# Kernel tuning notes

Hardware: AMD Instinct MI355X
Metric: run time of the kernel (lower is better)

The kernel has to match this reference:

```python
import jax, jax.numpy as jnp
import numpy as np

D = 1024
B, S_IMG, S_CTX = 2, 4096, 512
EPS = 1e-6


def rmsnorm(x, eps=1e-6):
    return x * jax.lax.rsqrt(jnp.mean(x * x, axis=-1, keepdims=True) + eps)


def layernorm(x, eps=1e-6):
    mu = jnp.mean(x, axis=-1, keepdims=True)
    var = jnp.mean((x - mu) ** 2, axis=-1, keepdims=True)
    return (x - mu) * jax.lax.rsqrt(var + eps)


def act_quant(x):
    # per-token 8-bit absmax quant
    scale = 127.0 / jnp.clip(jnp.max(jnp.abs(x), axis=-1, keepdims=True), 1e-5)
    return jnp.clip(jnp.round(x * scale), -128, 127) / scale


def weight_quant(w):
    # ternary (1.58-bit) absmean quant
    scale = 1.0 / jnp.clip(jnp.mean(jnp.abs(w)), 1e-5)
    return jnp.clip(jnp.round(w * scale), -1, 1) / scale


def bitlinear(x, w):
    # BitNet: RMSNorm -> STE activation quant, STE ternary weight quant
    xn = rmsnorm(x)
    xq = xn + jax.lax.stop_gradient(act_quant(xn) - xn)
    wq = w + jax.lax.stop_gradient(weight_quant(w) - w)
    return jnp.einsum('bsd,od->bso', xq, wq)


def ada_ln_zero(x, emb, w, b):
    e = (jax.nn.silu(emb) @ w.T + b)[:, None, :]  # [B,1,6D]
    scale_msa, shift_msa, gate_msa, scale_mlp, shift_mlp, gate_mlp = jnp.split(e, 6, axis=2)
    xn = layernorm(x) * (1.0 + scale_msa) + shift_msa
    return xn, gate_msa, shift_mlp, scale_mlp, gate_mlp


def hgrn_bit_attention(x, wi, wf, wg, wo, gnorm_w):
    i = bitlinear(x, wi)
    f = jax.nn.sigmoid(bitlinear(x, wf))
    i = jax.nn.silu(i) * (1.0 - f)  # swiglu(i, 1-f)
    # elementwise linear recurrence h_t = f_t * h_{t-1} + i_t over seq dim
    def step(h, xs):
        i_t, f_t = xs
        h = f_t * h + i_t
        return h, h
    _, o = jax.lax.scan(step, jnp.zeros_like(i[:, 0]), (i.transpose(1, 0, 2), f.transpose(1, 0, 2)))
    o = o.transpose(1, 0, 2)  # [B,S,D]
    g = bitlinear(x, wg)
    o = rmsnorm(o) * gnorm_w * (g * jax.nn.sigmoid(g))  # RMSNorm + swish gate
    return bitlinear(o, wo)


def bit_mlp(x, w_gate, w_down):
    y = bitlinear(x, w_gate)
    gate, y = jnp.split(y, 2, axis=-1)
    return bitlinear(jax.nn.silu(gate) * y, w_down)


def flux_block(hidden_states, encoder_hidden_states, temb,
               adaln_w, adaln_b, adaln_ctx_w, adaln_ctx_b,
               attn_wi, attn_wf, attn_wg, attn_wo, attn_gnorm_w,
               ff_wgate, ff_wdown, ffc_wgate, ffc_wdown):
    nh, gate_msa, shift_mlp, scale_mlp, gate_mlp = ada_ln_zero(hidden_states, temb, adaln_w, adaln_b)
    nc, c_gate_msa, c_shift_mlp, c_scale_mlp, c_gate_mlp = ada_ln_zero(encoder_hidden_states, temb, adaln_ctx_w, adaln_ctx_b)
    len_c = nc.shape[1]
    joint = jnp.concatenate([nc, nh], axis=1)
    attn_out = hgrn_bit_attention(joint, attn_wi, attn_wf, attn_wg, attn_wo, attn_gnorm_w)
    c_attn, x_attn = attn_out[:, :len_c], attn_out[:, len_c:]

    hidden_states = hidden_states + gate_msa * x_attn
    nh2 = layernorm(hidden_states) * (1.0 + scale_mlp) + shift_mlp
    hidden_states = hidden_states + gate_mlp * bit_mlp(nh2, ff_wgate, ff_wdown)

    encoder_hidden_states = encoder_hidden_states + c_gate_msa * c_attn
    nc2 = layernorm(encoder_hidden_states) * (1.0 + c_scale_mlp) + c_shift_mlp
    encoder_hidden_states = encoder_hidden_states + c_gate_mlp * bit_mlp(nc2, ffc_wgate, ffc_wdown)
    return hidden_states, encoder_hidden_states


def setup_inputs() -> dict:
    key = jax.random.key(0)
    ks = jax.random.split(key, 16)
    w = lambda k, shape: jax.random.normal(k, shape, jnp.float32) * 0.02
    return {
        'hidden_states': jax.random.normal(ks[0], (B, S_IMG, D), jnp.float32),
        'encoder_hidden_states': jax.random.normal(ks[1], (B, S_CTX, D), jnp.float32),
        'temb': jax.random.normal(ks[2], (B, D), jnp.float32),
        'adaln_w': w(ks[3], (6 * D, D)), 'adaln_b': jnp.zeros((6 * D,), jnp.float32),
        'adaln_ctx_w': w(ks[4], (6 * D, D)), 'adaln_ctx_b': jnp.zeros((6 * D,), jnp.float32),
        'attn_wi': w(ks[5], (D, D)), 'attn_wf': w(ks[6], (D, D)),
        'attn_wg': w(ks[7], (D, D)), 'attn_wo': w(ks[8], (D, D)),
        'attn_gnorm_w': jnp.ones((D,), jnp.float32),
        'ff_wgate': w(ks[9], (8 * D, D)), 'ff_wdown': w(ks[10], (D, 4 * D)),
        'ffc_wgate': w(ks[11], (8 * D, D)), 'ffc_wdown': w(ks[12], (D, 4 * D)),
    }


def reference(hidden_states, encoder_hidden_states, temb,
              adaln_w, adaln_b, adaln_ctx_w, adaln_ctx_b,
              attn_wi, attn_wf, attn_wg, attn_wo, attn_gnorm_w,
              ff_wgate, ff_wdown, ffc_wgate, ffc_wdown):
    return flux_block(hidden_states, encoder_hidden_states, temb,
                      adaln_w, adaln_b, adaln_ctx_w, adaln_ctx_b,
                      attn_wi, attn_wf, attn_wg, attn_wo, attn_gnorm_w,
                      ff_wgate, ff_wdown, ffc_wgate, ffc_wdown)
```

## Files before the change

kernel.cpp:

```cpp
#include <hip/hip_runtime.h>
#include <hip/hip_bf16.h>
#include <stdint.h>

#define DM   1024
#define SJ   4608
#define SCTX 512
#define SIMG 4096
#define NCH  512
#define TCH  9

typedef __attribute__((ext_vector_type(4))) int   i32x4;
typedef __attribute__((ext_vector_type(4))) float f32x4;

__device__ __forceinline__ float bf2f(unsigned short u){
  union { unsigned int i; float f; } v; v.i = ((unsigned int)u) << 16; return v.f;
}
__device__ __forceinline__ unsigned short f2bf(float f){
  unsigned int u = __float_as_uint(f);
  u += 0x7fffu + ((u >> 16) & 1u);
  return (unsigned short)(u >> 16);
}
__device__ __forceinline__ float sigm(float x){ return 1.f/(1.f+__expf(-x)); }
__device__ __forceinline__ signed char q8(float v, float lo, float hi){
  return (signed char)(int)fminf(fmaxf(rintf(v),lo),hi);
}

__device__ __forceinline__ float wsum(float v){
  #pragma unroll
  for(int o=32;o>0;o>>=1) v += __shfl_xor(v,o);
  return v;
}
__device__ __forceinline__ float wmax(float v){
  #pragma unroll
  for(int o=32;o>0;o>>=1) v = fmaxf(v,__shfl_xor(v,o));
  return v;
}
__device__ __forceinline__ void blockSumSum(float& a, float& b, float* s1, float* s2){
  a = wsum(a); b = wsum(b);
  if(!(threadIdx.x&63)){ s1[threadIdx.x>>6]=a; s2[threadIdx.x>>6]=b; }
  __syncthreads();
  a = s1[0]+s1[1]+s1[2]+s1[3];
  b = s2[0]+s2[1]+s2[2]+s2[3];
  __syncthreads();
}
__device__ __forceinline__ void blockSumMax(float& a, float& b, float* s1, float* s2){
  a = wsum(a); b = wmax(b);
  if(!(threadIdx.x&63)){ s1[threadIdx.x>>6]=a; s2[threadIdx.x>>6]=b; }
  __syncthreads();
  a = s1[0]+s1[1]+s1[2]+s1[3];
  b = fmaxf(fmaxf(s2[0],s2[1]),fmaxf(s2[2],s2[3]));
  __syncthreads();
}

typedef __attribute__((address_space(1))) void gvoid_t;
typedef __attribute__((address_space(3))) void lvoid_t;
__device__ __forceinline__ void gl_lds16(const void* g, void* l){
  __builtin_amdgcn_global_load_lds((gvoid_t*)g, (lvoid_t*)l, 16, 0, 0);
}

struct WList {
  const float* w[8];
  unsigned long long n[8];
  signed char* q[8];
};

__global__ __launch_bounds__(256)
void wq_reduce(WList L, float* __restrict__ part){
  __shared__ float s1[4];
  int m = blockIdx.y;
  const float4* w4 = (const float4*)L.w[m];
  size_t n4 = L.n[m] >> 2;
  float s = 0.f;
  for(size_t i = (size_t)blockIdx.x*256 + threadIdx.x; i < n4; i += (size_t)512*256){
    float4 v = w4[i];
    s += fabsf(v.x)+fabsf(v.y)+fabsf(v.z)+fabsf(v.w);
  }
  s = wsum(s);
  if(!(threadIdx.x&63)) s1[threadIdx.x>>6] = s;
  __syncthreads();
  if(!threadIdx.x) part[m*512 + blockIdx.x] = s1[0]+s1[1]+s1[2]+s1[3];
}

__global__ __launch_bounds__(256)
void wq_finalize(WList L, const float* __restrict__ part, float* __restrict__ swinv){
  __shared__ float s1[4];
  int m = blockIdx.x;
  float s = part[m*512 + threadIdx.x] + part[m*512 + 256 + threadIdx.x];
  s = wsum(s);
  if(!(threadIdx.x&63)) s1[threadIdx.x>>6] = s;
  __syncthreads();
  if(!threadIdx.x){
    float mean = (s1[0]+s1[1]+s1[2]+s1[3]) / (float)L.n[m];
    swinv[m] = fmaxf(mean, 1e-5f);
  }
}

__global__ __launch_bounds__(256)
void wq_quant(WList L, const float* __restrict__ swinv){
  int m = blockIdx.y;
  float sc = 1.f / swinv[m];
  const float4* w4 = (const float4*)L.w[m];
  signed char* q = L.q[m];
  size_t n4 = L.n[m] >> 2;
  for(size_t i = (size_t)blockIdx.x*256 + threadIdx.x; i < n4; i += (size_t)1024*256){
    float4 v = w4[i];
    char4 o;
    o.x = q8(v.x*sc,-1.f,1.f);
    o.y = q8(v.y*sc,-1.f,1.f);
    o.z = q8(v.z*sc,-1.f,1.f);
    o.w = q8(v.w*sc,-1.f,1.f);
    ((char4*)q)[i] = o;
  }
}

__global__ __launch_bounds__(256)
void adaln_gemv(const float* __restrict__ temb, const float* __restrict__ W,
                const float* __restrict__ bias, float* __restrict__ e){
  int o = blockIdx.x*4 + (threadIdx.x>>6);
  int b = blockIdx.y;
  int lane = threadIdx.x & 63;
  const float4* t4 = (const float4*)(temb + b*DM);
  const float4* w4 = (const float4*)(W + (size_t)o*DM);
  float acc = 0.f;
  #pragma unroll
  for(int i=0;i<4;i++){
    float4 tv = t4[i*64+lane], wv = w4[i*64+lane];
    acc += (tv.x*sigm(tv.x))*wv.x + (tv.y*sigm(tv.y))*wv.y
         + (tv.z*sigm(tv.z))*wv.z + (tv.w*sigm(tv.w))*wv.w;
  }
  acc = wsum(acc);
  if(!lane) e[b*6144 + o] = acc + bias[o];
}

__global__ __launch_bounds__(256)
void modnorm_quant(const float* __restrict__ x, int bshift,
                   const float* __restrict__ e, int scaleOff, int shiftOff,
                   signed char* __restrict__ xq, float* __restrict__ rsx,
                   int outRowOff, int outBatchStride){
  __shared__ float s1[4], s2[4];
  const int tid = threadIdx.x;
  const int row = blockIdx.x;
  const int b = row >> bshift, s = row & ((1<<bshift)-1);
  float4 xv = ((const float4*)(x + (size_t)row*DM))[tid];
  float sum = xv.x+xv.y+xv.z+xv.w;
  float ss  = xv.x*xv.x+xv.y*xv.y+xv.z*xv.z+xv.w*xv.w;
  blockSumSum(sum, ss, s1, s2);
  float mu  = sum * (1.f/DM);
  float inv = rsqrtf(ss*(1.f/DM) - mu*mu + 1e-6f);
  float4 scv = ((const float4*)(e + b*6144 + scaleOff))[tid];
  float4 shv = ((const float4*)(e + b*6144 + shiftOff))[tid];
  float n0 = (xv.x-mu)*inv*(1.f+scv.x)+shv.x;
  float n1 = (xv.y-mu)*inv*(1.f+scv.y)+shv.y;
  float n2 = (xv.z-mu)*inv*(1.f+scv.z)+shv.z;
  float n3 = (xv.w-mu)*inv*(1.f+scv.w)+shv.w;
  float ss2 = n0*n0+n1*n1+n2*n2+n3*n3;
  float mx  = fmaxf(fmaxf(fabsf(n0),fabsf(n1)),fmaxf(fabsf(n2),fabsf(n3)));
  blockSumMax(ss2, mx, s1, s2);
  float rms   = rsqrtf(ss2*(1.f/DM) + 1e-6f);
  float amaxn = fmaxf(mx*rms, 1e-5f);
  float k     = rms*127.f/amaxn;
  int orow = b*outBatchStride + outRowOff + s;
  char4 q;
  q.x = q8(n0*k,-128.f,127.f);
  q.y = q8(n1*k,-128.f,127.f);
  q.z = q8(n2*k,-128.f,127.f);
  q.w = q8(n3*k,-128.f,127.f);
  ((char4*)(xq + (size_t)orow*DM))[tid] = q;
  if(!tid) rsx[orow] = amaxn*(1.f/127.f);
}

__global__ __launch_bounds__(256)
void gnorm_quant(const unsigned short* __restrict__ o, const unsigned short* __restrict__ g,
                 const float* __restrict__ gnw,
                 signed char* __restrict__ xq, float* __restrict__ rsx){
  __shared__ float s1[4], s2[4];
  const int tid = threadIdx.x;
  const size_t row = blockIdx.x;
  ushort4 ov = ((const ushort4*)(o + row*DM))[tid];
  ushort4 gv = ((const ushort4*)(g + row*DM))[tid];
  float o0=bf2f(ov.x), o1=bf2f(ov.y), o2=bf2f(ov.z), o3=bf2f(ov.w);
  float g0=bf2f(gv.x), g1=bf2f(gv.y), g2=bf2f(gv.z), g3=bf2f(gv.w);
  float ss = o0*o0+o1*o1+o2*o2+o3*o3;
  float dummy = 0.f;
  blockSumSum(ss, dummy, s1, s2);
  float rms = rsqrtf(ss*(1.f/DM) + 1e-6f);
  float4 wv = ((const float4*)gnw)[tid];
  float n0 = o0*rms*wv.x*(g0*sigm(g0));
  float n1 = o1*rms*wv.y*(g1*sigm(g1));
  float n2 = o2*rms*wv.z*(g2*sigm(g2));
  float n3 = o3*rms*wv.w*(g3*sigm(g3));
  float ss2 = n0*n0+n1*n1+n2*n2+n3*n3;
  float mx  = fmaxf(fmaxf(fabsf(n0),fabsf(n1)),fmaxf(fabsf(n2),fabsf(n3)));
  blockSumMax(ss2, mx, s1, s2);
  float rms2  = rsqrtf(ss2*(1.f/DM) + 1e-6f);
  float amaxn = fmaxf(mx*rms2, 1e-5f);
  float k     = rms2*127.f/amaxn;
  char4 q;
  q.x = q8(n0*k,-128.f,127.f);
  q.y = q8(n1*k,-128.f,127.f);
  q.z = q8(n2*k,-128.f,127.f);
  q.w = q8(n3*k,-128.f,127.f);
  ((char4*)(xq + row*DM))[tid] = q;
  if(!tid) rsx[row] = amaxn*(1.f/127.f);
}

__global__ __launch_bounds__(256)
void rmsq4096(const unsigned short* __restrict__ z, signed char* __restrict__ zq,
              float* __restrict__ rsx){
  __shared__ float s1[4], s2[4];
  const int tid = threadIdx.x;
  const unsigned short* zr = z + (size_t)blockIdx.x*4096;
  signed char* qr = zq + (size_t)blockIdx.x*4096;
  float v[16];
  #pragma unroll
  for(int i=0;i<4;i++){
    ushort4 u = ((const ushort4*)zr)[tid + i*256];
    v[i*4+0]=bf2f(u.x); v[i*4+1]=bf2f(u.y); v[i*4+2]=bf2f(u.z); v[i*4+3]=bf2f(u.w);
  }
  float ss=0.f, mx=0.f;
  #pragma unroll
  for(int i=0;i<16;i++){ ss += v[i]*v[i]; mx = fmaxf(mx, fabsf(v[i])); }
  blockSumMax(ss, mx, s1, s2);
  float rms   = rsqrtf(ss*(1.f/4096.f) + 1e-6f);
  float amaxn = fmaxf(mx*rms, 1e-5f);
  float k     = rms*127.f/amaxn;
  #pragma unroll
  for(int i=0;i<4;i++){
    char4 q;
    q.x = q8(v[i*4+0]*k,-128.f,127.f);
    q.y = q8(v[i*4+1]*k,-128.f,127.f);
    q.z = q8(v[i*4+2]*k,-128.f,127.f);
    q.w = q8(v[i*4+3]*k,-128.f,127.f);
    ((char4*)qr)[tid + i*256] = q;
  }
  if(!tid) rsx[blockIdx.x] = amaxn*(1.f/127.f);
}

__global__ __launch_bounds__(256)
void scan_pass1(const unsigned short* __restrict__ ir, const unsigned short* __restrict__ fr,
                float* __restrict__ A, float* __restrict__ B){
  int c = blockIdx.x, b = blockIdx.y;
  int d0 = threadIdx.x*4;
  size_t base = ((size_t)b*SJ + (size_t)c*TCH)*DM + d0;
  float a0=1,a1=1,a2=1,a3=1, h0=0,h1=0,h2=0,h3=0;
  #pragma unroll
  for(int t=0;t<TCH;t++){
    ushort4 iv = *(const ushort4*)(ir + base + (size_t)t*DM);
    ushort4 fv = *(const ushort4*)(fr + base + (size_t)t*DM);
    float f0=sigm(bf2f(fv.x)), f1=sigm(bf2f(fv.y)), f2=sigm(bf2f(fv.z)), f3=sigm(bf2f(fv.w));
    float x0=bf2f(iv.x), x1=bf2f(iv.y), x2=bf2f(iv.z), x3=bf2f(iv.w);
    float p0=x0*sigm(x0)*(1.f-f0), p1=x1*sigm(x1)*(1.f-f1);
    float p2=x2*sigm(x2)*(1.f-f2), p3=x3*sigm(x3)*(1.f-f3);
    h0=f0*h0+p0; h1=f1*h1+p1; h2=f2*h2+p2; h3=f3*h3+p3;
    a0*=f0; a1*=f1; a2*=f2; a3*=f3;
  }
  size_t idx = (size_t)c*2048 + b*1024 + d0;
  *(float4*)(A + idx) = make_float4(a0,a1,a2,a3);
  *(float4*)(B + idx) = make_float4(h0,h1,h2,h3);
}

__global__ __launch_bounds__(256)
void scan_pass2(const float* __restrict__ A, const float* __restrict__ B, float* __restrict__ H){
  int chain = blockIdx.x*256 + threadIdx.x;
  float h = 0.f;
  for(int c0=0;c0<NCH;c0+=8){
    float a[8], bb[8];
    #pragma unroll
    for(int u=0;u<8;u++){
      a[u]  = A[(size_t)(c0+u)*2048 + chain];
      bb[u] = B[(size_t)(c0+u)*2048 + chain];
    }
    #pragma unroll
    for(int u=0;u<8;u++){
      H[(size_t)(c0+u)*2048 + chain] = h;
      h = a[u]*h + bb[u];
    }
  }
}

__global__ __launch_bounds__(256)
void scan_pass3(const unsigned short* __restrict__ ir, const unsigned short* __restrict__ fr,
                const float* __restrict__ H, unsigned short* __restrict__ o){
  int c = blockIdx.x, b = blockIdx.y;
  int d0 = threadIdx.x*4;
  size_t base = ((size_t)b*SJ + (size_t)c*TCH)*DM + d0;
  float4 hv = *(const float4*)(H + (size_t)c*2048 + b*1024 + d0);
  float h0=hv.x, h1=hv.y, h2=hv.z, h3=hv.w;
  #pragma unroll
  for(int t=0;t<TCH;t++){
    ushort4 iv = *(const ushort4*)(ir + base + (size_t)t*DM);
    ushort4 fv = *(const ushort4*)(fr + base + (size_t)t*DM);
    float f0=sigm(bf2f(fv.x)), f1=sigm(bf2f(fv.y)), f2=sigm(bf2f(fv.z)), f3=sigm(bf2f(fv.w));
    float x0=bf2f(iv.x), x1=bf2f(iv.y), x2=bf2f(iv.z), x3=bf2f(iv.w);
    float p0=x0*sigm(x0)*(1.f-f0), p1=x1*sigm(x1)*(1.f-f1);
    float p2=x2*sigm(x2)*(1.f-f2), p3=x3*sigm(x3)*(1.f-f3);
    h0=f0*h0+p0; h1=f1*h1+p1; h2=f2*h2+p2; h3=f3*h3+p3;
    ushort4 ov; ov.x=f2bf(h0); ov.y=f2bf(h1); ov.z=f2bf(h2); ov.w=f2bf(h3);
    *(ushort4*)(o + base + (size_t)t*DM) = ov;
  }
}

#define EPI_IFG    0
#define EPI_WO     1
#define EPI_GLU    2
#define EPI_RESID  3

struct GemmP {
  const float* rsx;
  const float* swinv;
  unsigned short* outb;
  float* outf;
  const float* resid;
  const float* egate;
  int bshift;
  const signed char* w2;
  const float* eh; const float* ec;
  const float* hid; const float* enc;
  float* out_h; float* out_c; float* out_c2;
};

template<int VAR, int EPI, int SWZ>
__global__ __launch_bounds__(512, 2)
void gemm8(const signed char* __restrict__ Aq, const signed char* __restrict__ Bq,
           int Ncols, int K, int lda, GemmP p){
  constexpr int BBYT = (VAR==2)? 16384 : 32768;
  constexpr int TB   = 32768 + BBYT;
  constexpr int NF   = (VAR==0)? 4 : 2;
  constexpr int BN   = (VAR==0)? 256 : 128;
  __shared__ char lds[2*TB];

  const int tid = threadIdx.x, wv = tid>>6, lane = tid&63;
  const int wm = wv>>2, wn = wv&3;
  const int nwg = gridDim.x*gridDim.y;
  const int id  = blockIdx.y*gridDim.x + blockIdx.x;
  int nb, mb;
  if constexpr (SWZ==1){
    const int x = id&7, j = id>>3;
    nb = x*4 + (j&3);
    mb = j>>2;
  } else {
    const int wg = (id&7)*(nwg>>3) + (id>>3);
    nb = wg % gridDim.x; mb = wg / gridDim.x;
  }

  const int srow = wv*8 + (lane>>3);
  const int sch  = ((lane&7) ^ (lane>>3))*16;
  const signed char* ag  = Aq + (size_t)(mb*256 + srow)*lda + sch;
  const signed char* bg1 = Bq + (size_t)(nb*BN  + srow)*lda + sch;
  const signed char* bg2 = nullptr;
  if constexpr (VAR==1) bg2 = p.w2 + (size_t)(nb*128 + srow)*lda + sch;
  const int wvoff = wv*1024;

  auto stageA = [&](char* bufn, int rb, int k0){
    gl_lds16(ag + (size_t)rb*lda + k0, bufn + rb*128 + wvoff);
  };
  auto stageB = [&](char* bufn, int rb, int k0, int m2){
    const signed char* src = m2 ? bg2 : bg1;
    gl_lds16(src + (size_t)rb*lda + k0, bufn + 32768 + m2*16384 + rb*128 + wvoff);
  };
  auto stagePh = [&](int ph, char* bufn, int kn){
    if constexpr (VAR==0){
      if(ph==0){ stageB(bufn,0,kn,0);   stageB(bufn,64,kn,0); }
      else if(ph==1){ stageB(bufn,128,kn,0); stageB(bufn,192,kn,0); }
      else if(ph==2){ stageA(bufn,0,kn);   stageA(bufn,128,kn); }
      else          { stageA(bufn,64,kn);  stageA(bufn,192,kn); }
    } else if constexpr (VAR==1){
      if(ph==0){ stageB(bufn,0,kn,0);  stageB(bufn,64,kn,0); }
      else if(ph==1){ stageB(bufn,0,kn,1);  stageB(bufn,64,kn,1); }
      else if(ph==2){ stageA(bufn,0,kn);   stageA(bufn,128,kn); }
      else          { stageA(bufn,64,kn);  stageA(bufn,192,kn); }
    } else {
      if(ph==0){ stageB(bufn,0,kn,0);  stageB(bufn,64,kn,0); }
      else if(ph==1){ stageA(bufn,0,kn);   stageA(bufn,128,kn); }
      else if(ph==2){ stageA(bufn,64,kn);  stageA(bufn,192,kn); }
    }
  };

  const int lr = lane&15;
  const int kq = lane>>4;
  const int axor = (lr&7)<<4;
  const int col0 = (kq<<4) ^ axor;
  const int col1 = (64 | (kq<<4)) ^ axor;
  const int arowb = (wm*128 + lr)*128;
  const int browb = ((VAR==0? wn*64 : wn*32) + lr)*128;

  i32x4 acc[8][NF];
  i32x4 acc2[(VAR==1)?8:1][NF];
  #pragma unroll
  for(int i=0;i<8;i++)
    #pragma unroll
    for(int j=0;j<NF;j++){ acc[i][j]=(i32x4){0,0,0,0}; if constexpr(VAR==1) acc2[i][j]=(i32x4){0,0,0,0}; }

  i32x4 breg[NF], breg2[(VAR==1)?NF:1];

  auto phase = [&](char* bufc, int ph, char* bufn, int kn, bool doStage){
    const int colb = (ph>>1)? col1 : col0;
    const int mh = ph&1;
    if(mh==0){
      #pragma unroll
      for(int nf=0;nf<NF;nf++)
        breg[nf] = *(const i32x4*)(bufc + 32768 + browb + nf*2048 + colb);
      if constexpr (VAR==1){
        #pragma unroll
        for(int nf=0;nf<NF;nf++)
          breg2[nf] = *(const i32x4*)(bufc + 32768 + 16384 + browb + nf*2048 + colb);
      }
    }
    i32x4 areg[4];
    #pragma unroll
    for(int i=0;i<4;i++)
      areg[i] = *(const i32x4*)(bufc + arowb + (mh*4+i)*2048 + colb);
    if(doStage) stagePh(ph, bufn, kn);
    __builtin_amdgcn_s_setprio(1);
    #pragma unroll
    for(int i=0;i<4;i++){
      #pragma unroll
      for(int nf=0;nf<NF;nf++){
        acc[mh*4+i][nf] = __builtin_amdgcn_mfma_i32_16x16x64_i8(areg[i], breg[nf], acc[mh*4+i][nf], 0,0,0);
        if constexpr (VAR==1)
          acc2[mh*4+i][nf] = __builtin_amdgcn_mfma_i32_16x16x64_i8(areg[i], breg2[nf], acc2[mh*4+i][nf], 0,0,0);
      }
    }
    __builtin_amdgcn_s_setprio(0);
  };

  #define VMW2 asm volatile("s_waitcnt vmcnt(2)" ::: "memory")
  #define VMW0 asm volatile("s_waitcnt vmcnt(0)" ::: "memory")
  #define BARR { __builtin_amdgcn_s_barrier(); __builtin_amdgcn_sched_barrier(0); }

  stagePh(0, lds, 0); stagePh(1, lds, 0); stagePh(2, lds, 0); stagePh(3, lds, 0);

  const int NT = K>>7;
  for(int t=0; t<NT-1; ++t){
    char* bufc = lds + (t&1)*TB;
    char* bufn = lds + ((t+1)&1)*TB;
    const int kn = (t+1)<<7;
    VMW2; BARR; phase(bufc, 0, bufn, kn, true);
    VMW2; BARR; phase(bufc, 1, bufn, kn, true);
          BARR; phase(bufc, 2, bufn, kn, true);
          BARR; phase(bufc, 3, bufn, kn, true);
  }
  {
    char* bufc = lds + ((NT-1)&1)*TB;
    VMW2; BARR; phase(bufc, 0, nullptr, 0, false);
    VMW0; BARR; phase(bufc, 1, nullptr, 0, false);
          BARR; phase(bufc, 2, nullptr, 0, false);
          BARR; phase(bufc, 3, nullptr, 0, false);
  }

  float sw;
  if constexpr (EPI==EPI_IFG) sw = p.swinv[(nb*256)>>10];
  else                        sw = *p.swinv;
  const int r0 = mb*256 + wm*128;
  const int c0 = nb*BN + wn*((VAR==0)?64:32);
  #pragma unroll
  for(int mf=0;mf<8;mf++){
    #pragma unroll
    for(int j=0;j<4;j++){
      int r = r0 + mf*16 + kq*4 + j;
      float rs = p.rsx[r]*sw;
      #pragma unroll
      for(int nf=0;nf<NF;nf++){
        int c = c0 + nf*16 + lr;
        float val = (float)acc[mf][nf][j]*rs;
        if constexpr (EPI==EPI_IFG){
          int mat = c >> 10;
          p.outb[(size_t)mat*9437184 + (size_t)r*1024 + (c&1023)] = f2bf(val);
        } else if constexpr (EPI==EPI_GLU){
          float v2 = (float)acc2[mf][nf][j]*rs;
          p.outb[(size_t)r*Ncols + c] = f2bf(val*sigm(val)*v2);
        } else if constexpr (EPI==EPI_RESID){
          int b = r >> p.bshift;
          size_t idx = (size_t)r*DM + c;
          p.outf[idx] = p.resid[idx] + p.egate[b*6144 + 5*1024 + c]*val;
        } else {
          int b = r / SJ; int s = r - b*SJ;
          if (s < SCTX){
            size_t idx = ((size_t)b*SCTX + s)*DM + c;
            float ov = p.enc[idx] + p.ec[b*6144 + 2*1024 + c]*val;
            p.out_c[idx]  = ov;
            p.out_c2[idx] = ov;
          } else {
            size_t idx = ((size_t)b*SIMG + (s-SCTX))*DM + c;
            p.out_h[idx] = p.hid[idx] + p.eh[b*6144 + 2*1024 + c]*val;
          }
        }
      }
    }
  }
  #undef VMW2
  #undef VMW0
  #undef BARR
}

__global__ __launch_bounds__(256, 2)
void gemm_ra8(const signed char* __restrict__ Aq, const signed char* __restrict__ Wq,
              int K, int lda, GemmP p){
  __shared__ signed char As[128*128];
  __shared__ signed char Bs[128*128];
  const int tid = threadIdx.x;
  const int wave = tid>>6, lane = tid&63;
  const int nwg = gridDim.x*gridDim.y;
  const int id  = blockIdx.y*gridDim.x + blockIdx.x;
  const int wg  = (id&7)*(nwg>>3) + (id>>3);
  const int nb  = wg % gridDim.x, mb = wg / gridDim.x;
  const int wr = wave>>1, wc = wave&1;
  const int koff = blockIdx.z*K;

  const int grow = wave*8 + (lane>>3);
  const int gcol = (lane&7)*16;
  const signed char* ag = Aq + (size_t)(mb*128 + grow)*lda + koff + gcol;
  const signed char* bg = Wq + (size_t)(nb*128 + grow)*lda + koff + gcol;
  char* asl = (char*)As + wave*1024;
  char* bsl = (char*)Bs + wave*1024;

  i32x4 acc[4][4];
  #pragma unroll
  for(int i=0;i<4;i++)
    #pragma unroll
    for(int j=0;j<4;j++) acc[i][j] = (i32x4){0,0,0,0};

  const int lrow = lane&15, kq = lane>>4;
  const signed char* arow = &As[(wr*64 + lrow)*128 + kq*16];
  const signed char* brow = &Bs[(wc*64 + lrow)*128 + kq*16];

  for(int k0=0; k0<K; k0+=128){
    #pragma unroll
    for(int pp=0;pp<4;pp++){
      gl_lds16(ag + (size_t)pp*32*lda + k0, asl + pp*4096);
      gl_lds16(bg + (size_t)pp*32*lda + k0, bsl + pp*4096);
    }
    __syncthreads();
    #pragma unroll
    for(int kk=0;kk<2;kk++){
      i32x4 af[4], bfr[4];
      #pragma unroll
      for(int m=0;m<4;m++) af[m]  = *(const i32x4*)(arow + m*2048 + kk*64);
      #pragma unroll
      for(int n=0;n<4;n++) bfr[n] = *(const i32x4*)(brow + n*2048 + kk*64);
      #pragma unroll
      for(int m=0;m<4;m++)
        #pragma unroll
        for(int n=0;n<4;n++)
          acc[m][n] = __builtin_amdgcn_mfma_i32_16x16x64_i8(af[m], bfr[n], acc[m][n], 0,0,0);
    }
    __syncthreads();
  }

  const float sw = *p.swinv;
  const int r0 = mb*128 + wr*64, c0 = nb*128 + wc*64;
  #pragma unroll
  for(int m=0;m<4;m++){
    #pragma unroll
    for(int j=0;j<4;j++){
      int r = r0 + m*16 + kq*4 + j;
      float rs = p.rsx[r]*sw;
      #pragma unroll
      for(int n=0;n<4;n++){
        int c = c0 + n*16 + lrow;
        float val = (float)acc[m][n][j]*rs;
        int b = r >> p.bshift;
        size_t idx = (size_t)r*DM + c;
        atomicAdd(&p.outf[idx], p.egate[b*6144 + 5*1024 + c]*val);
      }
    }
  }
}

extern "C" void kernel_launch(void* const* d_in, const int* in_sizes, int n_in,
                              void* d_out, int out_size, void* d_ws, size_t ws_size,
                              hipStream_t stream){
  (void)in_sizes; (void)n_in; (void)out_size; (void)ws_size;
  const float* hidden   = (const float*)d_in[0];
  const float* enc      = (const float*)d_in[1];
  const float* temb     = (const float*)d_in[2];
  const float* adaln_w  = (const float*)d_in[3];
  const float* adaln_b  = (const float*)d_in[4];
  const float* adaln_cw = (const float*)d_in[5];
  const float* adaln_cb = (const float*)d_in[6];
  const float* wi  = (const float*)d_in[7];
  const float* wf  = (const float*)d_in[8];
  const float* wg  = (const float*)d_in[9];
  const float* wo  = (const float*)d_in[10];
  const float* gnw = (const float*)d_in[11];
  const float* ffg = (const float*)d_in[12];
  const float* ffd = (const float*)d_in[13];
  const float* fcg = (const float*)d_in[14];
  const float* fcd = (const float*)d_in[15];

  const size_t MB = 1024ull*1024ull;
  char* ws = (char*)d_ws;
  signed char* W8_IFG = (signed char*)(ws + 0*MB);
  signed char* W8_WO  = (signed char*)(ws + 3*MB);
  signed char* W8_FFG = (signed char*)(ws + 4*MB);
  signed char* W8_FFD = (signed char*)(ws + 12*MB);
  signed char* W8_FCG = (signed char*)(ws + 16*MB);
  signed char* W8_FCD = (signed char*)(ws + 24*MB);
  float* PART  = (float*)(ws + 28*MB);
  float* SWINV = (float*)(ws + 28*MB + 32*1024);
  float* EH    = (float*)(ws + 28*MB + 64*1024);
  float* EC    = (float*)(ws + 28*MB + 112*1024);
  float* RSX1  = (float*)(ws + 28*MB + 160*1024);
  float* RSX2  = (float*)(ws + 28*MB + 200*1024);
  float* RSX3  = (float*)(ws + 28*MB + 240*1024);
  float* RSXZ  = (float*)(ws + 28*MB + 280*1024);
  float* RSX4  = (float*)(ws + 28*MB + 320*1024);
  float* RSXZC = (float*)(ws + 28*MB + 328*1024);
  float* SCANA = (float*)(ws + 29*MB);
  float* SCANB = (float*)(ws + 33*MB);
  float* SCANH = (float*)(ws + 37*MB);
  signed char* XQ8 = (signed char*)(ws + 41*MB);
  unsigned short* IRAW = (unsigned short*)(ws + 51*MB);
  unsigned short* FRAW = (unsigned short*)(ws + 69*MB);
  unsigned short* GRAW = (unsigned short*)(ws + 87*MB);
  unsigned short* OBUF = (unsigned short*)(ws + 105*MB);
  unsigned short* SGB  = (unsigned short*)(ws + 51*MB);
  signed char* SG8 = (signed char*)(ws + 115*MB);
  float* HNEW = (float*)(ws + 147*MB);
  float* CNEW = (float*)(ws + 181*MB);
  float* OUT_H = (float*)d_out;
  float* OUT_C = (float*)d_out + 8388608;

  WList L;
  L.w[0]=wi;  L.n[0]=1048576ull; L.q[0]=W8_IFG;
  L.w[1]=wf;  L.n[1]=1048576ull; L.q[1]=W8_IFG + 1048576;
  L.w[2]=wg;  L.n[2]=1048576ull; L.q[2]=W8_IFG + 2097152;
  L.w[3]=wo;  L.n[3]=1048576ull; L.q[3]=W8_WO;
  L.w[4]=ffg; L.n[4]=8388608ull; L.q[4]=W8_FFG;
  L.w[5]=ffd; L.n[5]=4194304ull; L.q[5]=W8_FFD;
  L.w[6]=fcg; L.n[6]=8388608ull; L.q[6]=W8_FCG;
  L.w[7]=fcd; L.n[7]=4194304ull; L.q[7]=W8_FCD;
  wq_reduce  <<<dim3(512,8), 256, 0, stream>>>(L, PART);
  wq_finalize<<<8,          256, 0, stream>>>(L, PART, SWINV);
  wq_quant   <<<dim3(1024,8),256, 0, stream>>>(L, SWINV);

  adaln_gemv<<<dim3(1536,2), 256, 0, stream>>>(temb, adaln_w,  adaln_b,  EH);
  adaln_gemv<<<dim3(1536,2), 256, 0, stream>>>(temb, adaln_cw, adaln_cb, EC);

  modnorm_quant<<<1024, 256, 0, stream>>>(enc,    9,  EC, 0, 1024, XQ8, RSX1, 0,   SJ);
  modnorm_quant<<<8192, 256, 0, stream>>>(hidden, 12, EH, 0, 1024, XQ8, RSX1, 512, SJ);

  GemmP p{};
  p.rsx = RSX1; p.swinv = SWINV; p.outb = IRAW;
  gemm8<0,EPI_IFG,0><<<dim3(12,36), 512, 0, stream>>>(XQ8, W8_IFG, 3072, 1024, 1024, p);

  scan_pass1<<<dim3(NCH,2), 256, 0, stream>>>(IRAW, FRAW, SCANA, SCANB);
  scan_pass2<<<8,           256, 0, stream>>>(SCANA, SCANB, SCANH);
  scan_pass3<<<dim3(NCH,2), 256, 0, stream>>>(IRAW, FRAW, SCANH, OBUF);

  gnorm_quant<<<9216, 256, 0, stream>>>(OBUF, GRAW, gnw, XQ8, RSX2);

  GemmP pw{};
  pw.rsx = RSX2; pw.swinv = SWINV+3;
  pw.eh = EH; pw.ec = EC; pw.hid = hidden; pw.enc = enc;
  pw.out_h = HNEW; pw.out_c = CNEW; pw.out_c2 = OUT_C;
  gemm8<2,EPI_WO,0><<<dim3(8,36), 512, 0, stream>>>(XQ8, W8_WO, 1024, 1024, 1024, pw);

  modnorm_quant<<<8192, 256, 0, stream>>>(HNEW, 12, EH, 3*1024, 4*1024, XQ8, RSX3, 0, SIMG);
  GemmP pg{};
  pg.rsx = RSX3; pg.swinv = SWINV+4; pg.outb = SGB; pg.w2 = W8_FFG + (size_t)4096*1024;
  gemm8<1,EPI_GLU,1><<<dim3(32,32), 512, 0, stream>>>(XQ8, W8_FFG, 4096, 1024, 1024, pg);
  rmsq4096<<<8192, 256, 0, stream>>>(SGB, SG8, RSXZ);
  GemmP pd{};
  pd.rsx = RSXZ; pd.swinv = SWINV+5; pd.outf = OUT_H; pd.resid = HNEW; pd.egate = EH; pd.bshift = 12;
  gemm8<2,EPI_RESID,0><<<dim3(8,32), 512, 0, stream>>>(SG8, W8_FFD, 1024, 4096, 4096, pd);

  modnorm_quant<<<1024, 256, 0, stream>>>(CNEW, 9, EC, 3*1024, 4*1024, XQ8, RSX4, 0, SCTX);
  GemmP pc{};
  pc.rsx = RSX4; pc.swinv = SWINV+6; pc.outb = SGB; pc.w2 = W8_FCG + (size_t)4096*1024;
  gemm8<1,EPI_GLU,1><<<dim3(32,4), 512, 0, stream>>>(XQ8, W8_FCG, 4096, 1024, 1024, pc);
  rmsq4096<<<1024, 256, 0, stream>>>(SGB, SG8, RSXZC);
  GemmP pe{};
  pe.rsx = RSXZC; pe.swinv = SWINV+7; pe.outf = OUT_C; pe.egate = EC; pe.bshift = 9;
  gemm_ra8<<<dim3(8,8,4), 256, 0, stream>>>(SG8, W8_FCD, 1024, 4096, pe);
}
```

Before: 511.4 us.

## Fuse gated RMSNorm into scan pass and move residual adds out of GEMM epilogues

The group-norm/swish-gate/quantization step now runs inside the final scan pass, so the bf16 scan output buffer is never written or reread. The Wo and FF-down GEMMs now write plain bf16 outputs. Their residual-plus-gate adds move into separate elementwise kernels, one of which also does the next adaLN modulated norm and quantization. This shortens the GEMM epilogues, which previously did scattered fp32 reads and writes. In exchange it adds extra bf16 intermediate traffic, two block reductions per timestep inside the scan kernel, and rounds the attention and MLP outputs to bf16 before the residual add.

```diff
diff --git a/kernel.cpp b/kernel.cpp
--- a/kernel.cpp
+++ b/kernel.cpp
@@ -170,38 +170,65 @@
 }
 
 __global__ __launch_bounds__(256)
-void gnorm_quant(const unsigned short* __restrict__ o, const unsigned short* __restrict__ g,
-                 const float* __restrict__ gnw,
-                 signed char* __restrict__ xq, float* __restrict__ rsx){
+void resid_modnorm(const float* __restrict__ x, const unsigned short* __restrict__ attn,
+                   int attnRowOff, int bshift,
+                   const float* __restrict__ e,
+                   float* __restrict__ hout,
+                   signed char* __restrict__ xq, float* __restrict__ rsx){
   __shared__ float s1[4], s2[4];
   const int tid = threadIdx.x;
-  const size_t row = blockIdx.x;
-  ushort4 ov = ((const ushort4*)(o + row*DM))[tid];
-  ushort4 gv = ((const ushort4*)(g + row*DM))[tid];
-  float o0=bf2f(ov.x), o1=bf2f(ov.y), o2=bf2f(ov.z), o3=bf2f(ov.w);
-  float g0=bf2f(gv.x), g1=bf2f(gv.y), g2=bf2f(gv.z), g3=bf2f(gv.w);
-  float ss = o0*o0+o1*o1+o2*o2+o3*o3;
-  float dummy = 0.f;
-  blockSumSum(ss, dummy, s1, s2);
-  float rms = rsqrtf(ss*(1.f/DM) + 1e-6f);
-  float4 wv = ((const float4*)gnw)[tid];
-  float n0 = o0*rms*wv.x*(g0*sigm(g0));
-  float n1 = o1*rms*wv.y*(g1*sigm(g1));
-  float n2 = o2*rms*wv.z*(g2*sigm(g2));
-  float n3 = o3*rms*wv.w*(g3*sigm(g3));
+  const int row = blockIdx.x;
+  const int b = row >> bshift, s = row & ((1<<bshift)-1);
+  const int arow = b*SJ + attnRowOff + s;
+  float4 xv = ((const float4*)(x + (size_t)row*DM))[tid];
+  ushort4 av = ((const ushort4*)(attn + (size_t)arow*DM))[tid];
+  float4 gv = ((const float4*)(e + b*6144 + 2*1024))[tid];
+  float h0 = xv.x + gv.x*bf2f(av.x);
+  float h1 = xv.y + gv.y*bf2f(av.y);
+  float h2 = xv.z + gv.z*bf2f(av.z);
+  float h3 = xv.w + gv.w*bf2f(av.w);
+  ((float4*)(hout + (size_t)row*DM))[tid] = make_float4(h0,h1,h2,h3);
+  float sum = h0+h1+h2+h3;
+  float ss  = h0*h0+h1*h1+h2*h2+h3*h3;
+  blockSumSum(sum, ss, s1, s2);
+  float mu  = sum * (1.f/DM);
+  float inv = rsqrtf(ss*(1.f/DM) - mu*mu + 1e-6f);
+  float4 scv = ((const float4*)(e + b*6144 + 3*1024))[tid];
+  float4 shv = ((const float4*)(e + b*6144 + 4*1024))[tid];
+  float n0 = (h0-mu)*inv*(1.f+scv.x)+shv.x;
+  float n1 = (h1-mu)*inv*(1.f+scv.y)+shv.y;
+  float n2 = (h2-mu)*inv*(1.f+scv.z)+shv.z;
+  float n3 = (h3-mu)*inv*(1.f+scv.w)+shv.w;
   float ss2 = n0*n0+n1*n1+n2*n2+n3*n3;
   float mx  = fmaxf(fmaxf(fabsf(n0),fabsf(n1)),fmaxf(fabsf(n2),fabsf(n3)));
   blockSumMax(ss2, mx, s1, s2);
-  float rms2  = rsqrtf(ss2*(1.f/DM) + 1e-6f);
-  float amaxn = fmaxf(mx*rms2, 1e-5f);
-  float k     = rms2*127.f/amaxn;
+  float rms   = rsqrtf(ss2*(1.f/DM) + 1e-6f);
+  float amaxn = fmaxf(mx*rms, 1e-5f);
+  float k     = rms*127.f/amaxn;
   char4 q;
   q.x = q8(n0*k,-128.f,127.f);
   q.y = q8(n1*k,-128.f,127.f);
   q.z = q8(n2*k,-128.f,127.f);
   q.w = q8(n3*k,-128.f,127.f);
-  ((char4*)(xq + row*DM))[tid] = q;
+  ((char4*)(xq + (size_t)row*DM))[tid] = q;
   if(!tid) rsx[row] = amaxn*(1.f/127.f);
+}
+
+__global__ __launch_bounds__(256)
+void resid_out(const float* __restrict__ hnew, const unsigned short* __restrict__ mlp,
+               const float* __restrict__ e, int bshift, float* __restrict__ out){
+  const int tid = threadIdx.x;
+  const int row = blockIdx.x;
+  const int b = row >> bshift;
+  float4 hv = ((const float4*)(hnew + (size_t)row*DM))[tid];
+  ushort4 mv = ((const ushort4*)(mlp + (size_t)row*DM))[tid];
+  float4 gv = ((const float4*)(e + b*6144 + 5*1024))[tid];
+  float4 o;
+  o.x = hv.x + gv.x*bf2f(mv.x);
+  o.y = hv.y + gv.y*bf2f(mv.y);
+  o.z = hv.z + gv.z*bf2f(mv.z);
+  o.w = hv.w + gv.w*bf2f(mv.w);
+  ((float4*)(out + (size_t)row*DM))[tid] = o;
 }
 
 __global__ __launch_bounds__(256)
@@ -279,13 +306,18 @@
 }
 
 __global__ __launch_bounds__(256)
-void scan_pass3(const unsigned short* __restrict__ ir, const unsigned short* __restrict__ fr,
-                const float* __restrict__ H, unsigned short* __restrict__ o){
+void scan3_gnorm(const unsigned short* __restrict__ ir, const unsigned short* __restrict__ fr,
+                 const float* __restrict__ H, const unsigned short* __restrict__ g,
+                 const float* __restrict__ gnw,
+                 signed char* __restrict__ xq, float* __restrict__ rsx){
+  __shared__ float s1[4], s2[4];
   int c = blockIdx.x, b = blockIdx.y;
-  int d0 = threadIdx.x*4;
+  const int tid = threadIdx.x;
+  int d0 = tid*4;
   size_t base = ((size_t)b*SJ + (size_t)c*TCH)*DM + d0;
   float4 hv = *(const float4*)(H + (size_t)c*2048 + b*1024 + d0);
   float h0=hv.x, h1=hv.y, h2=hv.z, h3=hv.w;
+  float4 wv = ((const float4*)gnw)[tid];
   #pragma unroll
   for(int t=0;t<TCH;t++){
     ushort4 iv = *(const ushort4*)(ir + base + (size_t)t*DM);
@@ -295,28 +327,44 @@
     float p0=x0*sigm(x0)*(1.f-f0), p1=x1*sigm(x1)*(1.f-f1);
     float p2=x2*sigm(x2)*(1.f-f2), p3=x3*sigm(x3)*(1.f-f3);
     h0=f0*h0+p0; h1=f1*h1+p1; h2=f2*h2+p2; h3=f3*h3+p3;
-    ushort4 ov; ov.x=f2bf(h0); ov.y=f2bf(h1); ov.z=f2bf(h2); ov.w=f2bf(h3);
-    *(ushort4*)(o + base + (size_t)t*DM) = ov;
+    float ss = h0*h0+h1*h1+h2*h2+h3*h3, dummy = 0.f;
+    blockSumSum(ss, dummy, s1, s2);
+    float rms = rsqrtf(ss*(1.f/DM) + 1e-6f);
+    ushort4 gv = *(const ushort4*)(g + base + (size_t)t*DM);
+    float g0=bf2f(gv.x), g1=bf2f(gv.y), g2=bf2f(gv.z), g3=bf2f(gv.w);
+    float n0 = h0*rms*wv.x*(g0*sigm(g0));
+    float n1 = h1*rms*wv.y*(g1*sigm(g1));
+    float n2 = h2*rms*wv.z*(g2*sigm(g2));
+    float n3 = h3*rms*wv.w*(g3*sigm(g3));
+    float ss2 = n0*n0+n1*n1+n2*n2+n3*n3;
+    float mx  = fmaxf(fmaxf(fabsf(n0),fabsf(n1)),fmaxf(fabsf(n2),fabsf(n3)));
+    blockSumMax(ss2, mx, s1, s2);
+    float rms2  = rsqrtf(ss2*(1.f/DM) + 1e-6f);
+    float amaxn = fmaxf(mx*rms2, 1e-5f);
+    float k     = rms2*127.f/amaxn;
+    char4 q;
+    q.x = q8(n0*k,-128.f,127.f);
+    q.y = q8(n1*k,-128.f,127.f);
+    q.z = q8(n2*k,-128.f,127.f);
+    q.w = q8(n3*k,-128.f,127.f);
+    size_t row = (size_t)b*SJ + (size_t)c*TCH + t;
+    *(char4*)(xq + row*DM + d0) = q;
+    if(!tid) rsx[row] = amaxn*(1.f/127.f);
   }
 }
 
 #define EPI_IFG    0
-#define EPI_WO     1
+#define EPI_OUT    1
 #define EPI_GLU    2
-#define EPI_RESID  3
 
 struct GemmP {
   const float* rsx;
   const float* swinv;
   unsigned short* outb;
   float* outf;
-  const float* resid;
   const float* egate;
   int bshift;
   const signed char* w2;
-  const float* eh; const float* ec;
-  const float* hid; const float* enc;
-  float* out_h; float* out_c; float* out_c2;
 };
 
 template<int VAR, int EPI, int SWZ>
@@ -469,21 +517,8 @@
         } else if constexpr (EPI==EPI_GLU){
           float v2 = (float)acc2[mf][nf][j]*rs;
           p.outb[(size_t)r*Ncols + c] = f2bf(val*sigm(val)*v2);
-        } else if constexpr (EPI==EPI_RESID){
-          int b = r >> p.bshift;
-          size_t idx = (size_t)r*DM + c;
-          p.outf[idx] = p.resid[idx] + p.egate[b*6144 + 5*1024 + c]*val;
         } else {
-          int b = r / SJ; int s = r - b*SJ;
-          if (s < SCTX){
-            size_t idx = ((size_t)b*SCTX + s)*DM + c;
-            float ov = p.enc[idx] + p.ec[b*6144 + 2*1024 + c]*val;
-            p.out_c[idx]  = ov;
-            p.out_c2[idx] = ov;
-          } else {
-            size_t idx = ((size_t)b*SIMG + (s-SCTX))*DM + c;
-            p.out_h[idx] = p.hid[idx] + p.eh[b*6144 + 2*1024 + c]*val;
-          }
+          p.outb[(size_t)r*Ncols + c] = f2bf(val);
         }
       }
     }
@@ -613,11 +648,11 @@
   unsigned short* IRAW = (unsigned short*)(ws + 51*MB);
   unsigned short* FRAW = (unsigned short*)(ws + 69*MB);
   unsigned short* GRAW = (unsigned short*)(ws + 87*MB);
-  unsigned short* OBUF = (unsigned short*)(ws + 105*MB);
-  unsigned short* SGB  = (unsigned short*)(ws + 51*MB);
-  signed char* SG8 = (signed char*)(ws + 115*MB);
-  float* HNEW = (float*)(ws + 147*MB);
-  float* CNEW = (float*)(ws + 181*MB);
+  unsigned short* ATTN = (unsigned short*)(ws + 51*MB);
+  signed char* SG8 = (signed char*)(ws + 51*MB);
+  unsigned short* MLPH = (unsigned short*)(ws + 83*MB);
+  float* HNEW = (float*)(ws + 105*MB);
+  unsigned short* SGB = (unsigned short*)(ws + 137*MB);
   float* OUT_H = (float*)d_out;
   float* OUT_C = (float*)d_out + 8388608;
 
@@ -646,29 +681,28 @@
 
   scan_pass1<<<dim3(NCH,2), 256, 0, stream>>>(IRAW, FRAW, SCANA, SCANB);
   scan_pass2<<<8,           256, 0, stream>>>(SCANA, SCANB, SCANH);
-  scan_pass3<<<dim3(NCH,2), 256, 0, stream>>>(IRAW, FRAW, SCANH, OBUF);
-
-  gnorm_quant<<<9216, 256, 0, stream>>>(OBUF, GRAW, gnw, XQ8, RSX2);
+  scan3_gnorm<<<dim3(NCH,2), 256, 0, stream>>>(IRAW, FRAW, SCANH, GRAW, gnw, XQ8, RSX2);
 
   GemmP pw{};
-  pw.rsx = RSX2; pw.swinv = SWINV+3;
-  pw.eh = EH; pw.ec = EC; pw.hid = hidden; pw.enc = enc;
-  pw.out_h = HNEW; pw.out_c = CNEW; pw.out_c2 = OUT_C;
-  gemm8<2,EPI_WO,0><<<dim3(8,36), 512, 0, stream>>>(XQ8, W8_WO, 1024, 1024, 1024, pw);
-
-  modnorm_quant<<<8192, 256, 0, stream>>>(HNEW, 12, EH, 3*1024, 4*1024, XQ8, RSX3, 0, SIMG);
+  pw.rsx = RSX2; pw.swinv = SWINV+3; pw.outb = ATTN;
+  gemm8<2,EPI_OUT,0><<<dim3(8,36), 512, 0, stream>>>(XQ8, W8_WO, 1024, 1024, 1024, pw);
+
+  resid_modnorm<<<8192, 256, 0, stream>>>(hidden, ATTN, 512, 12, EH, HNEW, XQ8, RSX3);
+  resid_modnorm<<<1024, 256, 0, stream>>>(enc,    ATTN, 0,   9,  EC, OUT_C,
+                                          XQ8 + (size_t)8192*1024, RSX4);
+
   GemmP pg{};
   pg.rsx = RSX3; pg.swinv = SWINV+4; pg.outb = SGB; pg.w2 = W8_FFG + (size_t)4096*1024;
   gemm8<1,EPI_GLU,1><<<dim3(32,32), 512, 0, stream>>>(XQ8, W8_FFG, 4096, 1024, 1024, pg);
   rmsq4096<<<8192, 256, 0, stream>>>(SGB, SG8, RSXZ);
   GemmP pd{};
-  pd.rsx = RSXZ; pd.swinv = SWINV+5; pd.outf = OUT_H; pd.resid = HNEW; pd.egate = EH; pd.bshift = 12;
-  gemm8<2,EPI_RESID,0><<<dim3(8,32), 512, 0, stream>>>(SG8, W8_FFD, 1024, 4096, 4096, pd);
-
-  modnorm_quant<<<1024, 256, 0, stream>>>(CNEW, 9, EC, 3*1024, 4*1024, XQ8, RSX4, 0, SCTX);
+  pd.rsx = RSXZ; pd.swinv = SWINV+5; pd.outb = MLPH;
+  gemm8<2,EPI_OUT,0><<<dim3(8,32), 512, 0, stream>>>(SG8, W8_FFD, 1024, 4096, 4096, pd);
+  resid_out<<<8192, 256, 0, stream>>>(HNEW, MLPH, EH, 12, OUT_H);
+
   GemmP pc{};
   pc.rsx = RSX4; pc.swinv = SWINV+6; pc.outb = SGB; pc.w2 = W8_FCG + (size_t)4096*1024;
-  gemm8<1,EPI_GLU,1><<<dim3(32,4), 512, 0, stream>>>(XQ8, W8_FCG, 4096, 1024, 1024, pc);
+  gemm8<1,EPI_GLU,1><<<dim3(32,4), 512, 0, stream>>>(XQ8 + (size_t)8192*1024, W8_FCG, 4096, 1024, 1024, pc);
   rmsq4096<<<1024, 256, 0, stream>>>(SGB, SG8, RSXZC);
   GemmP pe{};
   pe.rsx = RSXZC; pe.swinv = SWINV+7; pe.outf = OUT_C; pe.egate = EC; pe.bshift = 9;
```

Measured after the change: 465.4 us. 1.1x faster.
